# Kernel tuning notes

Measured on AMD Instinct MI355X. Metric: run time of the kernel, lower is better.

Reference implementation:

```python
import jax, jax.numpy as jnp
import numpy as np

B, S, D, H, E, K = 4, 2048, 1024, 2048, 8, 2


def setup_inputs() -> dict:
    key = jax.random.key(0)
    ks = jax.random.split(key, 6)
    s_d = 1.0 / np.sqrt(D)
    s_h = 1.0 / np.sqrt(H)
    return {
        "x": jax.random.normal(ks[0], (B, S, D), dtype=jnp.float32),
        "Wg": jax.random.normal(ks[1], (D, E), dtype=jnp.float32) * s_d,
        "bg": jnp.zeros((E,), dtype=jnp.float32),
        "w1": jax.random.normal(ks[2], (E, D, H), dtype=jnp.float32) * s_d,
        "w3": jax.random.normal(ks[3], (E, D, H), dtype=jnp.float32) * s_d,
        "w2": jax.random.normal(ks[4], (E, H, D), dtype=jnp.float32) * s_h,
    }


def reference(x, Wg, bg, w1, w3, w2):
    # Router (eval mode: no noise). logits: [B,S,E]
    logits = jnp.einsum("bsd,de->bse", x, Wg) + bg
    top_v, top_i = jax.lax.top_k(logits, K)          # [B,S,K]
    probs = jax.nn.softmax(top_v, axis=-1)           # softmax over -inf-masked logits == softmax over top-k
    # Scatter top-k probs back to dense gates [B,S,E] (zeros elsewhere)
    gates = jnp.sum(jax.nn.one_hot(top_i, E, dtype=x.dtype) * probs[..., None], axis=-2)
    # Combine: gate-weighted sum of per-expert SwiGLU FFN outputs.
    # gates[...,e] == 0 exactly for tokens not routed to expert e, matching the
    # original masked gather -> FFN -> weighted scatter-add.
    out = jnp.zeros_like(x)
    for e in range(E):
        h = jax.nn.silu(x @ w1[e]) * (x @ w3[e])     # [B,S,H]
        y = h @ w2[e]                                # [B,S,D]
        out = out + gates[..., e:e + 1] * y
    return out
```

## Files before the change

kernel.cpp:

```cpp
#include <hip/hip_runtime.h>

typedef short bf16x8 __attribute__((ext_vector_type(8)));
typedef float f32x4 __attribute__((ext_vector_type(4)));
typedef unsigned short u16;
typedef unsigned int u32;

#define TOKS 8192
#define DDIM 1024
#define HDIM 2048
#define NEXP 8
#define ROWS_TOTAL (2 * TOKS)

#define WL1_CAP 544
#define WL2_CAP 136

#define NSUB 32
#define SUBCAP 256
#define CSTRIDE 32

__device__ __forceinline__ u16 f2b(float f) {
  u32 x;
  __builtin_memcpy(&x, &f, 4);
  return (u16)((x + 0x7fffu + ((x >> 16) & 1u)) >> 16);
}

typedef const __attribute__((address_space(1))) u32* gp_t;
typedef __attribute__((address_space(3))) u32* lp_t;
__device__ __forceinline__ void glds16(const void* g, void* l) {
  __builtin_amdgcn_global_load_lds((gp_t)g, (lp_t)l, 16, 0, 0);
}

__global__ __launch_bounds__(256) void cvt_wT_kernel(const float* __restrict__ in,
                                                     u16* __restrict__ out, int K, int N) {
  size_t eo = (size_t)blockIdx.z * K * N;
  in += eo; out += eo;
  int n0 = blockIdx.x * 64, k0 = blockIdx.y * 64;
  __shared__ u16 s[64][72];
  int tid = threadIdx.x;
  int kr = tid >> 4, nc = (tid & 15) * 4;
#pragma unroll
  for (int i = 0; i < 4; ++i) {
    int k = k0 + i * 16 + kr;
    float4 v = *(const float4*)(in + (size_t)k * N + n0 + nc);
    ushort4 u;
    u.x = f2b(v.x); u.y = f2b(v.y); u.z = f2b(v.z); u.w = f2b(v.w);
    *(ushort4*)&s[i * 16 + kr][nc] = u;
  }
  __syncthreads();
  int nl = tid >> 2, kc = tid & 3;
  union { int4 v[2]; u16 u[16]; } o;
#pragma unroll
  for (int j = 0; j < 16; ++j) o.u[j] = s[kc * 16 + j][nl];
  u16* op = out + (size_t)(n0 + nl) * K + k0 + kc * 16;
  *(int4*)op = o.v[0];
  *(int4*)(op + 8) = o.v[1];
}

__global__ __launch_bounds__(256) void cvt_wc_kernel(const float* __restrict__ in,
                                                     u16* __restrict__ out, int K, int N,
                                                     int half) {
  in += (size_t)blockIdx.z * K * N;
  out += (size_t)blockIdx.z * 2 * K * N;
  int n0 = blockIdx.x * 64, k0 = blockIdx.y * 64;
  __shared__ u16 s[64][72];
  int tid = threadIdx.x;
  int kr = tid >> 4, nc = (tid & 15) * 4;
#pragma unroll
  for (int i = 0; i < 4; ++i) {
    int k = k0 + i * 16 + kr;
    float4 v = *(const float4*)(in + (size_t)k * N + n0 + nc);
    ushort4 u;
    u.x = f2b(v.x); u.y = f2b(v.y); u.z = f2b(v.z); u.w = f2b(v.w);
    *(ushort4*)&s[i * 16 + kr][nc] = u;
  }
  __syncthreads();
  int nl = tid >> 2, kc = tid & 3;
  union { int4 v[2]; u16 u[16]; } o;
#pragma unroll
  for (int j = 0; j < 16; ++j) o.u[j] = s[kc * 16 + j][nl];
  int n = n0 + nl;
  int orow = ((n >> 4) << 5) + half * 16 + (n & 15);
  u16* op = out + (size_t)orow * K + k0 + kc * 16;
  *(int4*)op = o.v[0];
  *(int4*)(op + 8) = o.v[1];
}

__global__ __launch_bounds__(256) void router_kernel(
    const float* __restrict__ x, const float* __restrict__ Wg,
    const float* __restrict__ bg, int* __restrict__ counts32,
    int* __restrict__ tok16, float* __restrict__ g16, u16* __restrict__ xb) {
  int lane = threadIdx.x & 63;
  int t = blockIdx.x * 4 + (threadIdx.x >> 6);
  int sub = blockIdx.x & (NSUB - 1);
  const float* xr = x + (size_t)t * DDIM;
  u16* xo = xb + (size_t)t * DDIM;
  float acc[NEXP];
#pragma unroll
  for (int e = 0; e < NEXP; ++e) acc[e] = 0.f;
#pragma unroll
  for (int jj = 0; jj < DDIM / 256; ++jj) {
    int d = jj * 256 + lane * 4;
    float4 xv = *(const float4*)(xr + d);
    ushort4 o;
    o.x = f2b(xv.x); o.y = f2b(xv.y); o.z = f2b(xv.z); o.w = f2b(xv.w);
    *(ushort4*)(xo + d) = o;
    float xs[4] = {xv.x, xv.y, xv.z, xv.w};
#pragma unroll
    for (int dd = 0; dd < 4; ++dd) {
      float4 w0 = *(const float4*)(Wg + (d + dd) * NEXP);
      float4 w1v = *(const float4*)(Wg + (d + dd) * NEXP + 4);
      acc[0] += xs[dd] * w0.x; acc[1] += xs[dd] * w0.y;
      acc[2] += xs[dd] * w0.z; acc[3] += xs[dd] * w0.w;
      acc[4] += xs[dd] * w1v.x; acc[5] += xs[dd] * w1v.y;
      acc[6] += xs[dd] * w1v.z; acc[7] += xs[dd] * w1v.w;
    }
  }
#pragma unroll
  for (int off = 32; off > 0; off >>= 1) {
#pragma unroll
    for (int e = 0; e < NEXP; ++e) acc[e] += __shfl_down(acc[e], off, 64);
  }
  if (lane == 0) {
    float v[NEXP];
#pragma unroll
    for (int e = 0; e < NEXP; ++e) v[e] = acc[e] + bg[e];
    int e0 = 0;
    float v0 = v[0];
#pragma unroll
    for (int e = 1; e < NEXP; ++e)
      if (v[e] > v0) { v0 = v[e]; e0 = e; }
    int e1 = -1;
    float v1 = -3.4e38f;
#pragma unroll
    for (int e = 0; e < NEXP; ++e)
      if (e != e0 && v[e] > v1) { v1 = v[e]; e1 = e; }
    if (e1 < 0) e1 = (e0 + 1) & 7;
    float ex = __expf(v1 - v0);
    float g0 = 1.f / (1.f + ex);
    float g1 = 1.f - g0;
    int c0 = sub * NEXP + e0;
    int s0 = atomicAdd(&counts32[c0 * CSTRIDE], 1);
    if (s0 < SUBCAP) { tok16[c0 * SUBCAP + s0] = t; g16[c0 * SUBCAP + s0] = g0; }
    int c1 = sub * NEXP + e1;
    int s1 = atomicAdd(&counts32[c1 * CSTRIDE], 1);
    if (s1 < SUBCAP) { tok16[c1 * SUBCAP + s1] = t; g16[c1 * SUBCAP + s1] = g1; }
  }
}

__global__ void offsets_kernel(const int* __restrict__ counts32, int* __restrict__ counts,
                               int* __restrict__ offsets, int* __restrict__ dstbase,
                               int* __restrict__ wl1, int* __restrict__ wl2) {
  int t = threadIdx.x;
  __shared__ int sc[NEXP];
  if (t < NEXP) {
    int c[NSUB];
#pragma unroll
    for (int sub = 0; sub < NSUB; ++sub) c[sub] = counts32[(sub * NEXP + t) * CSTRIDE];
    int run = 0;
#pragma unroll
    for (int sub = 0; sub < NSUB; ++sub) { dstbase[sub * NEXP + t] = run; run += c[sub]; }
    counts[t] = run;
    sc[t] = run;
  }
  __syncthreads();
  if (t == 0) {
    int o = 0;
    for (int e = 0; e < NEXP; ++e) { offsets[e] = o; o += sc[e]; }
    int j1 = 0, j2 = 0;
    for (int e = 0; e < NEXP; ++e) {
      int me = (sc[e] + 127) >> 7;
      for (int m = 0; m < me; ++m) {
        if (j1 + 4 <= WL1_CAP) {
#pragma unroll
          for (int yq = 0; yq < 4; ++yq) wl1[1 + j1 + yq] = (e << 8) | (m << 2) | yq;
          j1 += 4;
        }
        if (j2 < WL2_CAP) wl2[1 + j2++] = (e << 8) | m;
      }
    }
    wl1[0] = j1; wl2[0] = j2;
  }
}

__global__ __launch_bounds__(256) void compact_kernel(
    const int* __restrict__ counts32, const int* __restrict__ dstbase,
    const int* __restrict__ tok16, const float* __restrict__ g16,
    int* __restrict__ tok_ids, float* __restrict__ gates) {
  int idx = blockIdx.x;
  int e = idx & (NEXP - 1);
  int n = counts32[idx * CSTRIDE];
  if (n > SUBCAP) n = SUBCAP;
  int base = dstbase[idx];
  for (int i = threadIdx.x; i < n; i += 256) {
    tok_ids[e * TOKS + base + i] = tok16[idx * SUBCAP + i];
    gates[e * TOKS + base + i]   = g16[idx * SUBCAP + i];
  }
}

__global__ __launch_bounds__(256, 3) void ffn1_kernel(
    const u16* __restrict__ xb, const u16* __restrict__ wc,
    const int* __restrict__ tok_ids, const int* __restrict__ counts,
    const int* __restrict__ offsets, const int* __restrict__ wl,
    u16* __restrict__ h, int nbase_wc, int hw, int e_arg) {
  int e, m, y;
  if (e_arg >= 0) {
    e = e_arg; m = blockIdx.x; y = blockIdx.y;
    if (m * 128 >= counts[e]) return;
  } else {
    int bid = blockIdx.x;
    int xcd = bid & 7, j = bid >> 3;
    if (j >= wl[0]) return;
    int w = wl[1 + j];
    e = w >> 8; m = (w >> 2) & 63; y = xcd * 4 + (w & 3);
  }
  int count = counts[e];
  int mbase = m * 128;
  int row_off = (e_arg >= 0) ? 0 : offsets[e];
  int n0w = nbase_wc + y * 128;
  size_t we = (e_arg >= 0) ? 0 : (size_t)e;
  const u16* wce = wc + we * (size_t)(2 * HDIM * DDIM);

  __shared__ u16 sA[128 * 64];
  __shared__ u16 sB[128 * 64];
  __shared__ int stok[128];

  int tid = threadIdx.x, lane = tid & 63, wv = tid >> 6;
  if (tid < 128) {
    int s = mbase + tid;
    if (s >= count) s = count - 1;
    stok[tid] = tok_ids[e * TOKS + s];
  }
  __syncthreads();

  int rloc = lane >> 3, ch = lane & 7;
  u32 offA[4], offB[4];
#pragma unroll
  for (int i = 0; i < 4; ++i) {
    int r = (wv * 4 + i) * 8 + rloc;
    int sw = ch ^ (r & 7);
    offA[i] = (u32)stok[r] * DDIM + sw * 8;
    offB[i] = (u32)(n0w + r) * DDIM + sw * 8;
  }

  int wm = wv >> 1, wn = wv & 1;
  int rsel = lane & 15, q = lane >> 4;

  f32x4 acc[4][4];
#pragma unroll
  for (int i = 0; i < 4; ++i)
#pragma unroll
    for (int j = 0; j < 4; ++j) {
      f32x4 z = {0.f, 0.f, 0.f, 0.f};
      acc[i][j] = z;
    }

  for (int k0 = 0; k0 < DDIM; k0 += 64) {
    __syncthreads();
#pragma unroll
    for (int i = 0; i < 4; ++i) {
      int sbase = (wv * 4 + i) * 512;
      glds16(xb  + offA[i] + k0, sA + sbase);
      glds16(wce + offB[i] + k0, sB + sbase);
    }
    __syncthreads();

#pragma unroll
    for (int ks = 0; ks < 2; ++ks) {
      bf16x8 aF[4], bF[4];
#pragma unroll
      for (int mi = 0; mi < 4; ++mi) {
        int r = wm * 64 + mi * 16 + rsel;
        int p = (ks * 4 + q) ^ (r & 7);
        aF[mi] = *(const bf16x8*)&sA[r * 64 + p * 8];
      }
#pragma unroll
      for (int ni = 0; ni < 4; ++ni) {
        int r = wn * 64 + ni * 16 + rsel;
        int p = (ks * 4 + q) ^ (r & 7);
        bF[ni] = *(const bf16x8*)&sB[r * 64 + p * 8];
      }
#pragma unroll
      for (int mi = 0; mi < 4; ++mi)
#pragma unroll
        for (int ni = 0; ni < 4; ++ni)
          acc[mi][ni] = __builtin_amdgcn_mfma_f32_16x16x32_bf16(aF[mi], bF[ni], acc[mi][ni], 0, 0, 0);
    }
  }

  int cm = count - mbase;
#pragma unroll
  for (int mi = 0; mi < 4; ++mi) {
#pragma unroll
    for (int rr = 0; rr < 4; ++rr) {
      int mrow = wm * 64 + mi * 16 + q * 4 + rr;
      if (mrow < cm) {
#pragma unroll
        for (int np = 0; np < 2; ++np) {
          int hcol = y * 64 + (wn * 2 + np) * 16 + rsel;
          float u = acc[mi][2 * np][rr];
          float vv = acc[mi][2 * np + 1][rr];
          float hv = (u / (1.f + __expf(-u))) * vv;
          h[(size_t)(row_off + mbase + mrow) * hw + hcol] = f2b(hv);
        }
      }
    }
  }
}

__global__ __launch_bounds__(256) void ffn2_kernel(
    const u16* __restrict__ h, const u16* __restrict__ w2t,
    const int* __restrict__ tok_ids, const float* __restrict__ gates,
    const int* __restrict__ counts, const int* __restrict__ offsets,
    const int* __restrict__ wl, float* __restrict__ out, int kbase, int hw, int e_arg) {
  int e, m, y;
  if (e_arg >= 0) {
    e = e_arg; m = blockIdx.x; y = blockIdx.y;
    if (m * 128 >= counts[e]) return;
  } else {
    int bid = blockIdx.x;
    int xcd = bid & 7, j = bid >> 3;
    if (j >= wl[0]) return;
    int w = wl[1 + j];
    e = w >> 8; m = w & 63; y = xcd;
  }
  int count = counts[e];
  int mbase = m * 128;
  int row_off = (e_arg >= 0) ? 0 : offsets[e];
  int n0 = y * 128;
  size_t we = (e_arg >= 0) ? 0 : (size_t)e;
  const u16* w2e = w2t + we * (size_t)(HDIM * DDIM);

  __shared__ u16 sA[128 * 64];
  __shared__ u16 sB[128 * 64];
  __shared__ int stok[128];
  __shared__ float sg[128];

  int tid = threadIdx.x, lane = tid & 63, wv = tid >> 6;
  if (tid < 128) {
    int s = mbase + tid;
    if (s >= count) s = count - 1;
    stok[tid] = tok_ids[e * TOKS + s];
    sg[tid] = gates[e * TOKS + s];
  }
  __syncthreads();

  int rloc = lane >> 3, ch = lane & 7;
  u32 offA[4], offB[4];
#pragma unroll
  for (int i = 0; i < 4; ++i) {
    int r = (wv * 4 + i) * 8 + rloc;
    int sw = ch ^ (r & 7);
    int slot = mbase + r;
    if (slot >= count) slot = count - 1;
    offA[i] = (u32)(row_off + slot) * hw + sw * 8;
    offB[i] = (u32)(n0 + r) * HDIM + kbase + sw * 8;
  }

  int wm = wv >> 1, wn = wv & 1;
  int rsel = lane & 15, q = lane >> 4;

  f32x4 acc[4][4];
#pragma unroll
  for (int i = 0; i < 4; ++i)
#pragma unroll
    for (int j = 0; j < 4; ++j) {
      f32x4 z = {0.f, 0.f, 0.f, 0.f};
      acc[i][j] = z;
    }

  for (int k0 = 0; k0 < hw; k0 += 64) {
    __syncthreads();
#pragma unroll
    for (int i = 0; i < 4; ++i) {
      int sbase = (wv * 4 + i) * 512;
      glds16(h   + offA[i] + k0, sA + sbase);
      glds16(w2e + offB[i] + k0, sB + sbase);
    }
    __syncthreads();

#pragma unroll
    for (int ks = 0; ks < 2; ++ks) {
      bf16x8 aF[4], bF[4];
#pragma unroll
      for (int mi = 0; mi < 4; ++mi) {
        int r = wm * 64 + mi * 16 + rsel;
        int p = (ks * 4 + q) ^ (r & 7);
        aF[mi] = *(const bf16x8*)&sA[r * 64 + p * 8];
      }
#pragma unroll
      for (int ni = 0; ni < 4; ++ni) {
        int r = wn * 64 + ni * 16 + rsel;
        int p = (ks * 4 + q) ^ (r & 7);
        bF[ni] = *(const bf16x8*)&sB[r * 64 + p * 8];
      }
#pragma unroll
      for (int mi = 0; mi < 4; ++mi)
#pragma unroll
        for (int ni = 0; ni < 4; ++ni)
          acc[mi][ni] = __builtin_amdgcn_mfma_f32_16x16x32_bf16(aF[mi], bF[ni], acc[mi][ni], 0, 0, 0);
    }
  }

  int cm = count - mbase;
#pragma unroll
  for (int mi = 0; mi < 4; ++mi) {
#pragma unroll
    for (int rr = 0; rr < 4; ++rr) {
      int mrow = wm * 64 + mi * 16 + q * 4 + rr;
      if (mrow < cm) {
        int t = stok[mrow];
        float g = sg[mrow];
#pragma unroll
        for (int ni = 0; ni < 4; ++ni) {
          int col = n0 + wn * 64 + ni * 16 + rsel;
          atomicAdd(&out[(size_t)t * DDIM + col], g * acc[mi][ni][rr]);
        }
      }
    }
  }
}

extern "C" void kernel_launch(void* const* d_in, const int* in_sizes, int n_in,
                              void* d_out, int out_size, void* d_ws, size_t ws_size,
                              hipStream_t stream) {
  (void)in_sizes; (void)n_in; (void)out_size;
  const float* x  = (const float*)d_in[0];
  const float* Wg = (const float*)d_in[1];
  const float* bg = (const float*)d_in[2];
  const float* w1 = (const float*)d_in[3];
  const float* w3 = (const float*)d_in[4];
  const float* w2 = (const float*)d_in[5];
  float* out = (float*)d_out;

  char* ws = (char*)d_ws;
  int*   tok_ids  = (int*)ws;
  float* gates    = (float*)(ws + 262144);
  int*   counts   = (int*)(ws + 524288);
  int*   offsets  = (int*)(ws + 524352);
  int*   wl1      = (int*)(ws + 524416);
  int*   wl2      = (int*)(ws + 528512);
  int*   dstbase  = (int*)(ws + 529536);
  int*   counts32 = (int*)(ws + 532480);
  int*   tok16    = (int*)(ws + 565248);
  float* g16      = (float*)(ws + 827392);
  u16*   xb       = (u16*)(ws + (2 << 20));

  const size_t WEXP  = (size_t)HDIM * DDIM * 2;
  const size_t WALL  = 3ull * NEXP * WEXP;
  const size_t HFULL = (size_t)ROWS_TOTAL * HDIM * 2;
  const size_t base  = (2 << 20) + 16777216ull;

  hipMemsetAsync(counts32, 0, NEXP * NSUB * CSTRIDE * 4, stream);
  hipMemsetAsync(out, 0, (size_t)TOKS * DDIM * 4, stream);

  router_kernel<<<TOKS / 4, 256, 0, stream>>>(x, Wg, bg, counts32, tok16, g16, xb);
  offsets_kernel<<<1, 64, 0, stream>>>(counts32, counts, offsets, dstbase, wl1, wl2);
  compact_kernel<<<NSUB * NEXP, 256, 0, stream>>>(counts32, dstbase, tok16, g16,
                                                  tok_ids, gates);

  if (ws_size >= base + WALL + HFULL) {
    u16* wcb = (u16*)(ws + base);
    u16* w2t = wcb + (size_t)NEXP * 2 * HDIM * DDIM;
    u16* hb  = w2t + (size_t)NEXP * HDIM * DDIM;
    cvt_wc_kernel<<<dim3(HDIM / 64, DDIM / 64, NEXP), 256, 0, stream>>>(w1, wcb, DDIM, HDIM, 0);
    cvt_wc_kernel<<<dim3(HDIM / 64, DDIM / 64, NEXP), 256, 0, stream>>>(w3, wcb, DDIM, HDIM, 1);
    cvt_wT_kernel<<<dim3(DDIM / 64, HDIM / 64, NEXP), 256, 0, stream>>>(w2, w2t, HDIM, DDIM);
    ffn1_kernel<<<dim3(8 * WL1_CAP), 256, 0, stream>>>(
        xb, wcb, tok_ids, counts, offsets, wl1, hb, 0, HDIM, -1);
    ffn2_kernel<<<dim3(8 * WL2_CAP), 256, 0, stream>>>(
        hb, w2t, tok_ids, gates, counts, offsets, wl2, out, 0, HDIM, -1);
  } else {
    int hw = 128;
    const int cand[5] = {2048, 1024, 512, 256, 128};
    for (int i = 0; i < 5; ++i)
      if (base + 3 * WEXP + (size_t)TOKS * cand[i] * 2 <= ws_size) { hw = cand[i]; break; }
    u16* wcb = (u16*)(ws + base);
    u16* w2t = wcb + (size_t)2 * HDIM * DDIM;
    u16* hb  = w2t + (size_t)HDIM * DDIM;
    for (int e = 0; e < NEXP; ++e) {
      cvt_wc_kernel<<<dim3(HDIM / 64, DDIM / 64, 1), 256, 0, stream>>>(
          w1 + (size_t)e * DDIM * HDIM, wcb, DDIM, HDIM, 0);
      cvt_wc_kernel<<<dim3(HDIM / 64, DDIM / 64, 1), 256, 0, stream>>>(
          w3 + (size_t)e * DDIM * HDIM, wcb, DDIM, HDIM, 1);
      cvt_wT_kernel<<<dim3(DDIM / 64, HDIM / 64, 1), 256, 0, stream>>>(
          w2 + (size_t)e * HDIM * DDIM, w2t, HDIM, DDIM);
      for (int nb = 0; nb < HDIM; nb += hw) {
        ffn1_kernel<<<dim3(64, hw / 64, 1), 256, 0, stream>>>(
            xb, wcb, tok_ids, counts, offsets, nullptr, hb, 2 * nb, hw, e);
        ffn2_kernel<<<dim3(64, DDIM / 128, 1), 256, 0, stream>>>(
            hb, w2t, tok_ids, gates, counts, offsets, nullptr, out, nb, hw, e);
      }
    }
  }
}
```

Measured before the change: 580.8 us.

## Replace atomic scatter-add in FFN2 with row stores and a per-token combine kernel

```diff
diff --git a/kernel.cpp b/kernel.cpp
--- a/kernel.cpp
+++ b/kernel.cpp
@@ -184,17 +184,36 @@
 
 __global__ __launch_bounds__(256) void compact_kernel(
     const int* __restrict__ counts32, const int* __restrict__ dstbase,
+    const int* __restrict__ offsets,
     const int* __restrict__ tok16, const float* __restrict__ g16,
-    int* __restrict__ tok_ids, float* __restrict__ gates) {
+    int* __restrict__ tok_ids, float* __restrict__ gates,
+    int* __restrict__ posc, int* __restrict__ pos) {
   int idx = blockIdx.x;
   int e = idx & (NEXP - 1);
   int n = counts32[idx * CSTRIDE];
   if (n > SUBCAP) n = SUBCAP;
   int base = dstbase[idx];
+  int eoff = offsets[e];
   for (int i = threadIdx.x; i < n; i += 256) {
-    tok_ids[e * TOKS + base + i] = tok16[idx * SUBCAP + i];
+    int t = tok16[idx * SUBCAP + i];
+    tok_ids[e * TOKS + base + i] = t;
     gates[e * TOKS + base + i]   = g16[idx * SUBCAP + i];
-  }
+    int slot = atomicAdd(&posc[t], 1);
+    if (slot < 2) pos[t * 2 + slot] = eoff + base + i;
+  }
+}
+
+__global__ __launch_bounds__(256) void combine_kernel(
+    const float* __restrict__ y2, const int* __restrict__ pos,
+    float* __restrict__ out) {
+  int t = blockIdx.x;
+  int r0 = pos[2 * t], r1 = pos[2 * t + 1];
+  int c = threadIdx.x * 4;
+  float4 a = *(const float4*)(y2 + (size_t)r0 * DDIM + c);
+  float4 b = *(const float4*)(y2 + (size_t)r1 * DDIM + c);
+  float4 o;
+  o.x = a.x + b.x; o.y = a.y + b.y; o.z = a.z + b.z; o.w = a.w + b.w;
+  *(float4*)(out + (size_t)t * DDIM + c) = o;
 }
 
 __global__ __launch_bounds__(256, 3) void ffn1_kernel(
@@ -311,7 +330,8 @@
     const u16* __restrict__ h, const u16* __restrict__ w2t,
     const int* __restrict__ tok_ids, const float* __restrict__ gates,
     const int* __restrict__ counts, const int* __restrict__ offsets,
-    const int* __restrict__ wl, float* __restrict__ out, int kbase, int hw, int e_arg) {
+    const int* __restrict__ wl, float* __restrict__ out,
+    float* __restrict__ y2, int kbase, int hw, int e_arg) {
   int e, m, y;
   if (e_arg >= 0) {
     e = e_arg; m = blockIdx.x; y = blockIdx.y;
@@ -408,12 +428,21 @@
     for (int rr = 0; rr < 4; ++rr) {
       int mrow = wm * 64 + mi * 16 + q * 4 + rr;
       if (mrow < cm) {
-        int t = stok[mrow];
         float g = sg[mrow];
-#pragma unroll
-        for (int ni = 0; ni < 4; ++ni) {
-          int col = n0 + wn * 64 + ni * 16 + rsel;
-          atomicAdd(&out[(size_t)t * DDIM + col], g * acc[mi][ni][rr]);
+        if (y2) {
+          size_t rbase = (size_t)(row_off + mbase + mrow) * DDIM;
+#pragma unroll
+          for (int ni = 0; ni < 4; ++ni) {
+            int col = n0 + wn * 64 + ni * 16 + rsel;
+            y2[rbase + col] = g * acc[mi][ni][rr];
+          }
+        } else {
+          int t = stok[mrow];
+#pragma unroll
+          for (int ni = 0; ni < 4; ++ni) {
+            int col = n0 + wn * 64 + ni * 16 + rsel;
+            atomicAdd(&out[(size_t)t * DDIM + col], g * acc[mi][ni][rr]);
+          }
         }
       }
     }
@@ -443,32 +472,49 @@
   int*   counts32 = (int*)(ws + 532480);
   int*   tok16    = (int*)(ws + 565248);
   float* g16      = (float*)(ws + 827392);
+  int*   posc     = (int*)(ws + 1089536);
+  int*   pos      = (int*)(ws + 1122304);
   u16*   xb       = (u16*)(ws + (2 << 20));
 
   const size_t WEXP  = (size_t)HDIM * DDIM * 2;
   const size_t WALL  = 3ull * NEXP * WEXP;
   const size_t HFULL = (size_t)ROWS_TOTAL * HDIM * 2;
+  const size_t Y2SZ  = (size_t)ROWS_TOTAL * DDIM * 4;
   const size_t base  = (2 << 20) + 16777216ull;
 
   hipMemsetAsync(counts32, 0, NEXP * NSUB * CSTRIDE * 4, stream);
-  hipMemsetAsync(out, 0, (size_t)TOKS * DDIM * 4, stream);
+  hipMemsetAsync(posc, 0, TOKS * 4, stream);
 
   router_kernel<<<TOKS / 4, 256, 0, stream>>>(x, Wg, bg, counts32, tok16, g16, xb);
   offsets_kernel<<<1, 64, 0, stream>>>(counts32, counts, offsets, dstbase, wl1, wl2);
-  compact_kernel<<<NSUB * NEXP, 256, 0, stream>>>(counts32, dstbase, tok16, g16,
-                                                  tok_ids, gates);
-
-  if (ws_size >= base + WALL + HFULL) {
+  compact_kernel<<<NSUB * NEXP, 256, 0, stream>>>(counts32, dstbase, offsets, tok16, g16,
+                                                  tok_ids, gates, posc, pos);
+
+  if (ws_size >= base + WALL + HFULL + Y2SZ) {
     u16* wcb = (u16*)(ws + base);
     u16* w2t = wcb + (size_t)NEXP * 2 * HDIM * DDIM;
     u16* hb  = w2t + (size_t)NEXP * HDIM * DDIM;
+    float* y2 = (float*)(hb + (size_t)ROWS_TOTAL * HDIM);
     cvt_wc_kernel<<<dim3(HDIM / 64, DDIM / 64, NEXP), 256, 0, stream>>>(w1, wcb, DDIM, HDIM, 0);
     cvt_wc_kernel<<<dim3(HDIM / 64, DDIM / 64, NEXP), 256, 0, stream>>>(w3, wcb, DDIM, HDIM, 1);
     cvt_wT_kernel<<<dim3(DDIM / 64, HDIM / 64, NEXP), 256, 0, stream>>>(w2, w2t, HDIM, DDIM);
     ffn1_kernel<<<dim3(8 * WL1_CAP), 256, 0, stream>>>(
         xb, wcb, tok_ids, counts, offsets, wl1, hb, 0, HDIM, -1);
     ffn2_kernel<<<dim3(8 * WL2_CAP), 256, 0, stream>>>(
-        hb, w2t, tok_ids, gates, counts, offsets, wl2, out, 0, HDIM, -1);
+        hb, w2t, tok_ids, gates, counts, offsets, wl2, out, y2, 0, HDIM, -1);
+    combine_kernel<<<TOKS, 256, 0, stream>>>(y2, pos, out);
+  } else if (ws_size >= base + WALL + HFULL) {
+    u16* wcb = (u16*)(ws + base);
+    u16* w2t = wcb + (size_t)NEXP * 2 * HDIM * DDIM;
+    u16* hb  = w2t + (size_t)NEXP * HDIM * DDIM;
+    hipMemsetAsync(out, 0, (size_t)TOKS * DDIM * 4, stream);
+    cvt_wc_kernel<<<dim3(HDIM / 64, DDIM / 64, NEXP), 256, 0, stream>>>(w1, wcb, DDIM, HDIM, 0);
+    cvt_wc_kernel<<<dim3(HDIM / 64, DDIM / 64, NEXP), 256, 0, stream>>>(w3, wcb, DDIM, HDIM, 1);
+    cvt_wT_kernel<<<dim3(DDIM / 64, HDIM / 64, NEXP), 256, 0, stream>>>(w2, w2t, HDIM, DDIM);
+    ffn1_kernel<<<dim3(8 * WL1_CAP), 256, 0, stream>>>(
+        xb, wcb, tok_ids, counts, offsets, wl1, hb, 0, HDIM, -1);
+    ffn2_kernel<<<dim3(8 * WL2_CAP), 256, 0, stream>>>(
+        hb, w2t, tok_ids, gates, counts, offsets, wl2, out, nullptr, 0, HDIM, -1);
   } else {
     int hw = 128;
     const int cand[5] = {2048, 1024, 512, 256, 128};
@@ -477,6 +523,7 @@
     u16* wcb = (u16*)(ws + base);
     u16* w2t = wcb + (size_t)2 * HDIM * DDIM;
     u16* hb  = w2t + (size_t)HDIM * DDIM;
+    hipMemsetAsync(out, 0, (size_t)TOKS * DDIM * 4, stream);
     for (int e = 0; e < NEXP; ++e) {
       cvt_wc_kernel<<<dim3(HDIM / 64, DDIM / 64, 1), 256, 0, stream>>>(
           w1 + (size_t)e * DDIM * HDIM, wcb, DDIM, HDIM, 0);
@@ -488,8 +535,8 @@
         ffn1_kernel<<<dim3(64, hw / 64, 1), 256, 0, stream>>>(
             xb, wcb, tok_ids, counts, offsets, nullptr, hb, 2 * nb, hw, e);
         ffn2_kernel<<<dim3(64, DDIM / 128, 1), 256, 0, stream>>>(
-            hb, w2t, tok_ids, gates, counts, offsets, nullptr, out, nb, hw, e);
-      }
-    }
-  }
-}
+            hb, w2t, tok_ids, gates, counts, offsets, nullptr, out, nullptr, nb, hw, e);
+      }
+    }
+  }
+}
```

After: 555.5 us. 1.05x faster.
